# Kernel optimization log

Measured on AMD Instinct MI355X. Metric: run time of the kernel, lower is better.

## Reference

```python
import jax, jax.numpy as jnp
import numpy as np

B, V, CIN, H, W = 2, 4, 256, 96, 96
COUT, VS = 32, 64


def setup_inputs() -> dict:
    key = jax.random.key(0)
    k1, k2, k3, k4, k5 = jax.random.split(key, 5)
    features = jax.random.normal(k1, (B, V, CIN, H, W), dtype=jnp.float32)
    proj_matricies = jax.random.normal(k2, (B, V, 3, 4), dtype=jnp.float32)
    coord_volumes = jax.random.normal(k3, (B, VS, VS, VS, 3), dtype=jnp.float32) * 1000.0
    W_proc = jax.random.normal(k4, (COUT, CIN), dtype=jnp.float32) * 0.05
    b_proc = jax.random.normal(k5, (COUT,), dtype=jnp.float32) * 0.01
    return {"features": features, "proj_matricies": proj_matricies,
            "coord_volumes": coord_volumes, "W_proc": W_proc, "b_proc": b_proc}


def _bilinear_sample(feat, x, y):
    # feat: [C, H, W]; x, y: [N] pixel coords (align_corners=True mapping already applied)
    Hh, Ww = feat.shape[1], feat.shape[2]
    x0 = jnp.floor(x).astype(jnp.int32); x1 = x0 + 1
    y0 = jnp.floor(y).astype(jnp.int32); y1 = y0 + 1
    wx1 = x - x0; wx0 = 1.0 - wx1
    wy1 = y - y0; wy0 = 1.0 - wy1

    def gather(xi, yi):
        valid = ((xi >= 0) & (xi < Ww) & (yi >= 0) & (yi < Hh)).astype(feat.dtype)
        xc = jnp.clip(xi, 0, Ww - 1); yc = jnp.clip(yi, 0, Hh - 1)
        return feat[:, yc, xc] * valid  # [C, N] (zeros padding)

    return (gather(x0, y0) * (wx0 * wy0)
            + gather(x1, y0) * (wx1 * wy0)
            + gather(x0, y1) * (wx0 * wy1)
            + gather(x1, y1) * (wx1 * wy1))


def reference(features, proj_matricies, coord_volumes, W_proc, b_proc):
    b, v, cin, h, w = features.shape
    vs = coord_volumes.shape[1]
    # 1x1 conv (process_feature)
    feats = jnp.einsum('bvchw,oc->bvohw', features, W_proc) + b_proc[None, None, :, None, None]
    c = feats.shape[2]
    # homogeneous 3D grid points: [B, N, 4]
    pts = coord_volumes.reshape(b, -1, 3)
    pts_h = jnp.concatenate([pts, jnp.ones(pts.shape[:-1] + (1,), pts.dtype)], axis=-1)
    # project to image plane: [B, V, N, 3] homogeneous (u, v, w)
    proj_pts = jnp.einsum('bvij,bnj->bvni', proj_matricies, pts_h)
    wz = proj_pts[..., 2]
    invalid = wz <= 0.0
    wz_safe = jnp.where(wz == 0.0, 1.0, wz)
    u = proj_pts[..., 0] / wz_safe
    ve = proj_pts[..., 1] / wz_safe
    # normalized grid coords (faithful to original: x divided by feature_shape[0]=H, y by feature_shape[1]=W)
    gx = 2.0 * (u / h - 0.5)
    gy = 2.0 * (ve / w - 0.5)
    # align_corners=True pixel coords: x indexes width, y indexes height
    px = (gx + 1.0) * 0.5 * (w - 1)
    py = (gy + 1.0) * 0.5 * (h - 1)
    # sample per (batch, view): [B, V, C, N]
    sampled = jax.vmap(jax.vmap(_bilinear_sample))(feats, px, py)
    sampled = jnp.where(invalid[:, :, None, :], 0.0, sampled)
    # softmax over views per (b, c, voxel), weighted sum
    weights = jax.nn.softmax(sampled, axis=1)
    vol = jnp.sum(sampled * weights, axis=1)  # [B, C, N]
    return vol.reshape(b, c, vs, vs, vs)
```

## Files before the change

kernel.cpp:

```cpp
#include <hip/hip_runtime.h>
#include <hip/hip_bf16.h>

#define CIN   256
#define COUT  32
#define IMG_H 96
#define IMG_W 96
#define HW    (IMG_H*IMG_W)
#define NB    2
#define NV    4
#define VSZ   64
#define NVOX  (VSZ*VSZ*VSZ)

__global__ __launch_bounds__(256) void conv1x1_kernel(
    const float* __restrict__ features,
    const float* __restrict__ Wp,
    const float* __restrict__ bp,
    __hip_bfloat16* __restrict__ out)
{
    const int og   = __builtin_amdgcn_readfirstlane((threadIdx.x >> 6) & 3);
    const int lane = threadIdx.x & 63;
    const int bv   = blockIdx.y;
    const int px   = blockIdx.x*64 + lane;
    const float* f     = features + (size_t)bv*CIN*HW + px;
    const float* wbase = Wp + (size_t)og*8*CIN;

    float acc[8];
    #pragma unroll
    for (int j = 0; j < 8; ++j) acc[j] = bp[og*8 + j];

    for (int cc = 0; cc < CIN; cc += 8) {
        float x[8];
        #pragma unroll
        for (int i = 0; i < 8; ++i)
            x[i] = f[(size_t)(cc + i)*HW];
        #pragma unroll
        for (int i = 0; i < 8; ++i) {
            #pragma unroll
            for (int j = 0; j < 8; ++j)
                acc[j] += x[i] * wbase[(size_t)j*CIN + cc + i];
        }
    }

    union { uint4 u4; __hip_bfloat16 h[8]; } pk;
    #pragma unroll
    for (int j = 0; j < 8; ++j) pk.h[j] = __float2bfloat16(acc[j]);
    *(uint4*)(out + ((size_t)(bv*HW + px))*COUT + og*8) = pk.u4;
}

__global__ __launch_bounds__(256) void volgen_kernel(
    const __hip_bfloat16* __restrict__ feats,
    const float* __restrict__ proj,
    const float* __restrict__ coords,
    float* __restrict__ out)
{
    __shared__ float T[COUT*65];
    const int tid = threadIdx.x;
    const int vl  = tid >> 2;
    const int cg  = tid & 3;
    const int b   = blockIdx.y;
    const int n   = blockIdx.x*64 + vl;

    const float* cp = coords + ((size_t)b*NVOX + n)*3;
    const float X = cp[0], Y = cp[1], Z = cp[2];

    int   off[NV][4];
    float wgt[NV][4];
    #pragma unroll
    for (int v = 0; v < NV; ++v) {
        const float* P = proj + (size_t)(b*NV + v)*12;
        const float wz = P[8]*X + P[9]*Y + P[10]*Z + P[11];
        const bool  vz = wz > 0.f;
        const float rz = __builtin_amdgcn_rcpf(wz);
        float px = (P[0]*X + P[1]*Y + P[2]*Z + P[3]) * rz * (95.f/96.f);
        float py = (P[4]*X + P[5]*Y + P[6]*Z + P[7]) * rz * (95.f/96.f);
        px = vz ? px : 0.f;  py = vz ? py : 0.f;
        px = fminf(fmaxf(px, -1.0e6f), 1.0e6f);
        py = fminf(fmaxf(py, -1.0e6f), 1.0e6f);
        const float fx0 = floorf(px), fy0 = floorf(py);
        const int x0 = (int)fx0, y0 = (int)fy0, x1 = x0+1, y1 = y0+1;
        const float wx1 = px - fx0, wx0 = 1.f - wx1;
        const float wy1 = py - fy0, wy0 = 1.f - wy1;
        const bool vx0 = (unsigned)x0 < (unsigned)IMG_W;
        const bool vx1 = (unsigned)x1 < (unsigned)IMG_W;
        const bool vy0 = (unsigned)y0 < (unsigned)IMG_H;
        const bool vy1 = (unsigned)y1 < (unsigned)IMG_H;
        const int cx0 = min(max(x0, 0), IMG_W-1), cx1 = min(max(x1, 0), IMG_W-1);
        const int cy0 = min(max(y0, 0), IMG_H-1), cy1 = min(max(y1, 0), IMG_H-1);
        const int base = ((b*NV + v)*HW)*COUT + cg*8;
        off[v][0] = base + (cy0*IMG_W + cx0)*COUT;  wgt[v][0] = (vz & vx0 & vy0) ? wx0*wy0 : 0.f;
        off[v][1] = base + (cy0*IMG_W + cx1)*COUT;  wgt[v][1] = (vz & vx1 & vy0) ? wx1*wy0 : 0.f;
        off[v][2] = base + (cy1*IMG_W + cx0)*COUT;  wgt[v][2] = (vz & vx0 & vy1) ? wx0*wy1 : 0.f;
        off[v][3] = base + (cy1*IMG_W + cx1)*COUT;  wgt[v][3] = (vz & vx1 & vy1) ? wx1*wy1 : 0.f;
    }

    uint4 t[NV][4];
    #pragma unroll
    for (int v = 0; v < NV; ++v)
        #pragma unroll
        for (int c = 0; c < 4; ++c)
            t[v][c] = *(const uint4*)(feats + off[v][c]);

    float A[8], Bs[8];
    #pragma unroll
    for (int j = 0; j < 8; ++j) { A[j] = 0.f; Bs[j] = 0.f; }

    #pragma unroll
    for (int v = 0; v < NV; ++v) {
        float s[8];
        #pragma unroll
        for (int j = 0; j < 8; ++j) s[j] = 0.f;
        #pragma unroll
        for (int c = 0; c < 4; ++c) {
            const float w = wgt[v][c];
            const unsigned tu[4] = { t[v][c].x, t[v][c].y, t[v][c].z, t[v][c].w };
            #pragma unroll
            for (int k = 0; k < 4; ++k) {
                s[2*k]   += w * __uint_as_float(tu[k] << 16);
                s[2*k+1] += w * __uint_as_float(tu[k] & 0xffff0000u);
            }
        }
        #pragma unroll
        for (int j = 0; j < 8; ++j) {
            const float e = __expf(s[j]);
            A[j] += e;  Bs[j] += s[j]*e;
        }
    }

    #pragma unroll
    for (int j = 0; j < 8; ++j)
        T[(cg*8 + j)*65 + vl] = Bs[j] * __builtin_amdgcn_rcpf(A[j]);
    __syncthreads();

    const size_t ob = (size_t)b*COUT*NVOX + (size_t)blockIdx.x*64;
    #pragma unroll
    for (int i = 0; i < 8; ++i) {
        const int idx = i*256 + tid;
        const int ch = idx >> 6, vx = idx & 63;
        out[ob + (size_t)ch*NVOX + vx] = T[ch*65 + vx];
    }
}

extern "C" void kernel_launch(void* const* d_in, const int* in_sizes, int n_in,
                              void* d_out, int out_size, void* d_ws, size_t ws_size,
                              hipStream_t stream)
{
    const float* features = (const float*)d_in[0];
    const float* proj     = (const float*)d_in[1];
    const float* coords   = (const float*)d_in[2];
    const float* Wp       = (const float*)d_in[3];
    const float* bp       = (const float*)d_in[4];
    float* out = (float*)d_out;
    __hip_bfloat16* featsT = (__hip_bfloat16*)d_ws;

    hipLaunchKernelGGL(conv1x1_kernel, dim3(HW/64, NB*NV), dim3(256), 0, stream,
                       features, Wp, bp, featsT);
    hipLaunchKernelGGL(volgen_kernel, dim3(NVOX/64, NB), dim3(256), 0, stream,
                       featsT, proj, coords, out);
}
```

Before: 188.9 us.

## Compute all conv outputs per thread and share projection work via LDS

The 1x1 conv kernel now has each thread compute all 32 output channels. Before, four wavefronts each computed 8 channels and each re-read the same input pixels, so input feature traffic was repeated. The volume kernel now computes projection offsets and bilinear weights once per (voxel, view) and shares them through shared memory. Before, each of the four channel-group threads redundantly projected all four views. The cost is higher register pressure in the conv kernel (32 accumulators plus 16 inputs), fewer conv blocks' worth of threads, and an extra barrier in the volume kernel.

```diff
diff --git a/kernel.cpp b/kernel.cpp
--- a/kernel.cpp
+++ b/kernel.cpp
@@ -11,40 +11,40 @@
 #define VSZ   64
 #define NVOX  (VSZ*VSZ*VSZ)
 
-__global__ __launch_bounds__(256) void conv1x1_kernel(
+__global__ __launch_bounds__(64) void conv1x1_kernel(
     const float* __restrict__ features,
     const float* __restrict__ Wp,
     const float* __restrict__ bp,
     __hip_bfloat16* __restrict__ out)
 {
-    const int og   = __builtin_amdgcn_readfirstlane((threadIdx.x >> 6) & 3);
-    const int lane = threadIdx.x & 63;
+    const int lane = threadIdx.x;
     const int bv   = blockIdx.y;
     const int px   = blockIdx.x*64 + lane;
-    const float* f     = features + (size_t)bv*CIN*HW + px;
-    const float* wbase = Wp + (size_t)og*8*CIN;
+    const float* f = features + (size_t)bv*CIN*HW + px;
 
-    float acc[8];
+    float acc[COUT];
     #pragma unroll
-    for (int j = 0; j < 8; ++j) acc[j] = bp[og*8 + j];
+    for (int j = 0; j < COUT; ++j) acc[j] = bp[j];
 
-    for (int cc = 0; cc < CIN; cc += 8) {
-        float x[8];
+    for (int cc = 0; cc < CIN; cc += 16) {
+        float x[16];
         #pragma unroll
-        for (int i = 0; i < 8; ++i)
+        for (int i = 0; i < 16; ++i)
             x[i] = f[(size_t)(cc + i)*HW];
         #pragma unroll
-        for (int i = 0; i < 8; ++i) {
+        for (int i = 0; i < 16; ++i) {
             #pragma unroll
-            for (int j = 0; j < 8; ++j)
-                acc[j] += x[i] * wbase[(size_t)j*CIN + cc + i];
+            for (int j = 0; j < COUT; ++j)
+                acc[j] += x[i] * Wp[(size_t)j*CIN + cc + i];
         }
     }
 
-    union { uint4 u4; __hip_bfloat16 h[8]; } pk;
+    union { uint4 u4[4]; __hip_bfloat16 h[COUT]; } pk;
     #pragma unroll
-    for (int j = 0; j < 8; ++j) pk.h[j] = __float2bfloat16(acc[j]);
-    *(uint4*)(out + ((size_t)(bv*HW + px))*COUT + og*8) = pk.u4;
+    for (int j = 0; j < COUT; ++j) pk.h[j] = __float2bfloat16(acc[j]);
+    uint4* op = (uint4*)(out + ((size_t)(bv*HW + px))*COUT);
+    #pragma unroll
+    for (int k = 0; k < 4; ++k) op[k] = pk.u4[k];
 }
 
 __global__ __launch_bounds__(256) void volgen_kernel(
@@ -53,21 +53,21 @@
     const float* __restrict__ coords,
     float* __restrict__ out)
 {
+    __shared__ int   OffL[NV][64][4];
+    __shared__ float WgtL[NV][64][4];
     __shared__ float T[COUT*65];
+
     const int tid = threadIdx.x;
-    const int vl  = tid >> 2;
-    const int cg  = tid & 3;
     const int b   = blockIdx.y;
-    const int n   = blockIdx.x*64 + vl;
 
-    const float* cp = coords + ((size_t)b*NVOX + n)*3;
-    const float X = cp[0], Y = cp[1], Z = cp[2];
+    {
+        const int vox  = tid >> 2;
+        const int view = tid & 3;
+        const int n    = blockIdx.x*64 + vox;
+        const float* cp = coords + ((size_t)b*NVOX + n)*3;
+        const float X = cp[0], Y = cp[1], Z = cp[2];
+        const float* P = proj + (size_t)(b*NV + view)*12;
 
-    int   off[NV][4];
-    float wgt[NV][4];
-    #pragma unroll
-    for (int v = 0; v < NV; ++v) {
-        const float* P = proj + (size_t)(b*NV + v)*12;
         const float wz = P[8]*X + P[9]*Y + P[10]*Z + P[11];
         const bool  vz = wz > 0.f;
         const float rz = __builtin_amdgcn_rcpf(wz);
@@ -86,19 +86,25 @@
         const bool vy1 = (unsigned)y1 < (unsigned)IMG_H;
         const int cx0 = min(max(x0, 0), IMG_W-1), cx1 = min(max(x1, 0), IMG_W-1);
         const int cy0 = min(max(y0, 0), IMG_H-1), cy1 = min(max(y1, 0), IMG_H-1);
-        const int base = ((b*NV + v)*HW)*COUT + cg*8;
-        off[v][0] = base + (cy0*IMG_W + cx0)*COUT;  wgt[v][0] = (vz & vx0 & vy0) ? wx0*wy0 : 0.f;
-        off[v][1] = base + (cy0*IMG_W + cx1)*COUT;  wgt[v][1] = (vz & vx1 & vy0) ? wx1*wy0 : 0.f;
-        off[v][2] = base + (cy1*IMG_W + cx0)*COUT;  wgt[v][2] = (vz & vx0 & vy1) ? wx0*wy1 : 0.f;
-        off[v][3] = base + (cy1*IMG_W + cx1)*COUT;  wgt[v][3] = (vz & vx1 & vy1) ? wx1*wy1 : 0.f;
+        const int base = (b*NV + view)*HW*(COUT*2);
+        int4 of;
+        of.x = base + (cy0*IMG_W + cx0)*(COUT*2);
+        of.y = base + (cy0*IMG_W + cx1)*(COUT*2);
+        of.z = base + (cy1*IMG_W + cx0)*(COUT*2);
+        of.w = base + (cy1*IMG_W + cx1)*(COUT*2);
+        float4 wg;
+        wg.x = (vz & vx0 & vy0) ? wx0*wy0 : 0.f;
+        wg.y = (vz & vx1 & vy0) ? wx1*wy0 : 0.f;
+        wg.z = (vz & vx0 & vy1) ? wx0*wy1 : 0.f;
+        wg.w = (vz & vx1 & vy1) ? wx1*wy1 : 0.f;
+        *(int4*)  (&OffL[view][vox][0]) = of;
+        *(float4*)(&WgtL[view][vox][0]) = wg;
     }
+    __syncthreads();
 
-    uint4 t[NV][4];
-    #pragma unroll
-    for (int v = 0; v < NV; ++v)
-        #pragma unroll
-        for (int c = 0; c < 4; ++c)
-            t[v][c] = *(const uint4*)(feats + off[v][c]);
+    const int vl = tid >> 2;
+    const int cg = tid & 3;
+    const char* fb = (const char*)feats + cg*16;
 
     float A[8], Bs[8];
     #pragma unroll
@@ -106,17 +112,28 @@
 
     #pragma unroll
     for (int v = 0; v < NV; ++v) {
+        const int4   of = *(const int4*)  (&OffL[v][vl][0]);
+        const float4 wg = *(const float4*)(&WgtL[v][vl][0]);
+        const uint4 t0 = *(const uint4*)(fb + of.x);
+        const uint4 t1 = *(const uint4*)(fb + of.y);
+        const uint4 t2 = *(const uint4*)(fb + of.z);
+        const uint4 t3 = *(const uint4*)(fb + of.w);
+
         float s[8];
         #pragma unroll
         for (int j = 0; j < 8; ++j) s[j] = 0.f;
-        #pragma unroll
-        for (int c = 0; c < 4; ++c) {
-            const float w = wgt[v][c];
-            const unsigned tu[4] = { t[v][c].x, t[v][c].y, t[v][c].z, t[v][c].w };
+        {
+            const uint4* ts[4] = { &t0, &t1, &t2, &t3 };
+            const float  ws[4] = { wg.x, wg.y, wg.z, wg.w };
             #pragma unroll
-            for (int k = 0; k < 4; ++k) {
-                s[2*k]   += w * __uint_as_float(tu[k] << 16);
-                s[2*k+1] += w * __uint_as_float(tu[k] & 0xffff0000u);
+            for (int c = 0; c < 4; ++c) {
+                const float w = ws[c];
+                const unsigned tu[4] = { ts[c]->x, ts[c]->y, ts[c]->z, ts[c]->w };
+                #pragma unroll
+                for (int k = 0; k < 4; ++k) {
+                    s[2*k]   += w * __uint_as_float(tu[k] << 16);
+                    s[2*k+1] += w * __uint_as_float(tu[k] & 0xffff0000u);
+                }
             }
         }
         #pragma unroll
@@ -152,7 +169,7 @@
     float* out = (float*)d_out;
     __hip_bfloat16* featsT = (__hip_bfloat16*)d_ws;
 
-    hipLaunchKernelGGL(conv1x1_kernel, dim3(HW/64, NB*NV), dim3(256), 0, stream,
+    hipLaunchKernelGGL(conv1x1_kernel, dim3(HW/64, NB*NV), dim3(64), 0, stream,
                        features, Wp, bp, featsT);
     hipLaunchKernelGGL(volgen_kernel, dim3(NVOX/64, NB), dim3(256), 0, stream,
                        featsT, proj, coords, out);
```

Result: slower. 331.8 us (+75.6%).
